# Optimization experiments

Measured on AMD Instinct MI355X. Metric: run time of the kernel, lower is better.

Reference implementation:

```python
import jax, jax.numpy as jnp
import numpy as np

ALPHA = 1.0

def setup_inputs() -> dict:
    key = jax.random.key(0)
    k1, k2, k3, k4 = jax.random.split(key, 4)
    B, N, D = 2048, 32768, 128
    return {
        "anchor": jax.random.normal(k1, (B, D), dtype=jnp.float32),
        "positive": jax.random.normal(k2, (B, D), dtype=jnp.float32),
        "negative": jax.random.normal(k3, (N, D), dtype=jnp.float32),
        "r_score": jax.random.normal(k4, (B, 1), dtype=jnp.float32),
    }

def reference(anchor, positive, negative, r_score):
    # pos_sim: [B,1] elementwise dot per row
    pos_sim = jnp.sum(anchor * positive, axis=1, keepdims=True)
    # neg_mul: [B,N] score matrix; row-wise stable logsumexp -> [B,1]
    neg_mul = jnp.matmul(anchor, negative.T)
    neg_sim = jax.scipy.special.logsumexp(neg_mul, axis=1, keepdims=True)
    loss = jax.nn.relu(neg_sim - pos_sim + r_score + ALPHA)
    return jnp.mean(loss)
```

## Files before the change

kernel.cpp:

```cpp
#include <hip/hip_runtime.h>
#include <hip/hip_bf16.h>


#define B_ROWS 2048
#define N_NEG  32768
#define DIM    128
#define LOG2E  1.4426950408889634f
#define LN2    0.6931471805599453f

typedef __bf16 bf16x8 __attribute__((ext_vector_type(8)));
typedef float  f32x4  __attribute__((ext_vector_type(4)));

static __device__ inline unsigned short f2bf(float f) {
    union { float f; unsigned u; } v; v.f = f;
    unsigned r = v.u + 0x7FFF + ((v.u >> 16) & 1);
    return (unsigned short)(r >> 16);
}

static __device__ inline void load_lds16(const void* g, void* s) {
    __builtin_amdgcn_global_load_lds(
        (const __attribute__((address_space(1))) void*)g,
        (__attribute__((address_space(3))) void*)s,
        16, 0, 0);
}

__global__ void prep(const float* __restrict__ anchor,
                     const float* __restrict__ positive,
                     const float* __restrict__ neg,
                     unsigned short* __restrict__ a_bf,
                     unsigned short* __restrict__ n_bf,
                     float* __restrict__ pos_sim,
                     float* __restrict__ sumexp) {
    int t = threadIdx.x;
    if (blockIdx.x < 256) {
        int row = blockIdx.x * 8 + (t >> 5);
        int c4  = (t & 31) * 4;
        const float4 a4 = *(const float4*)(anchor   + row * DIM + c4);
        const float4 p4 = *(const float4*)(positive + row * DIM + c4);
        float dot = a4.x * p4.x + a4.y * p4.y + a4.z * p4.z + a4.w * p4.w;
        ushort4 ab;
        ab.x = f2bf(a4.x * LOG2E); ab.y = f2bf(a4.y * LOG2E);
        ab.z = f2bf(a4.z * LOG2E); ab.w = f2bf(a4.w * LOG2E);
        *(ushort4*)(a_bf + row * DIM + c4) = ab;
        #pragma unroll
        for (int m = 1; m <= 16; m <<= 1) dot += __shfl_xor(dot, m, 64);
        if ((t & 31) == 0) { pos_sim[row] = dot; sumexp[row] = 0.0f; }
    } else {
        int i = (blockIdx.x - 256) * 256 + t;
        #pragma unroll
        for (int k = 0; k < 4; k++) {
            int idx = i + k * (1024 * 256);
            float4 v = *(const float4*)(neg + (size_t)idx * 4);
            ushort4 o;
            o.x = f2bf(v.x); o.y = f2bf(v.y); o.z = f2bf(v.z); o.w = f2bf(v.w);
            *(ushort4*)(n_bf + (size_t)idx * 4) = o;
        }
    }
}

#define CHUNK 1024
#define TSTEPS (CHUNK / 128)

__global__ __launch_bounds__(256, 2) void fused_gemm_lse(
        const unsigned short* __restrict__ A,
        const unsigned short* __restrict__ Nb,
        float* __restrict__ sumexp) {
    __shared__ unsigned short lds[4 * 8192];

    const int bid     = blockIdx.x;
    const int rowTile = bid & 15;
    const int chunk   = bid >> 4;
    const int wave = threadIdx.x >> 6, lane = threadIdx.x & 63;
    const int wr = wave >> 1, wc = wave & 1;
    const int q = lane >> 4, c = lane & 15;
    const int lrow = lane >> 4;
    const int lchk = lane & 15;

    const unsigned short* Ag = A + rowTile * (128 * DIM);
    const unsigned short* Bg = Nb + (size_t)(chunk * CHUNK) * DIM;

#define STAGE_TILE(gbase, tt)                                                  \
    {                                                                          \
        const int h_ = wave >> 1;                                              \
        const int s_ = (2 * (tt) + 2 + h_) & 3;                                \
        _Pragma("unroll")                                                      \
        for (int i_ = 0; i_ < 8; i_++) {                                       \
            int rloc_ = (wave & 1) * 32 + i_ * 4;        \
            int rg_   = h_ * 64 + rloc_ + lrow;         \
            int gofs_ = rg_ * DIM + ((lchk ^ (rg_ & 7)) << 3);                 \
            load_lds16((gbase) + gofs_, &lds[s_ * 8192 + rloc_ * DIM]);        \
        }                                                                      \
    }

    STAGE_TILE(Ag, -1);
    STAGE_TILE(Bg, 0);
    asm volatile("s_waitcnt vmcnt(8)" ::: "memory");
    __builtin_amdgcn_s_barrier();

    int swz[4];
    #pragma unroll
    for (int k = 0; k < 4; k++) swz[k] = (((k * 4 + q) ^ (c & 7)) << 3);

    bf16x8 af[4][4];
    #pragma unroll
    for (int i = 0; i < 4; i++) {
        int row = i * 16 + c;
        #pragma unroll
        for (int k = 0; k < 4; k++)
            af[i][k] = *(const bf16x8*)&lds[wr * 8192 + row * DIM + swz[k]];
    }
    asm volatile("s_waitcnt lgkmcnt(0)" ::: "memory");
    __builtin_amdgcn_s_barrier();

    STAGE_TILE(Bg + 128 * DIM, 1);

    const f32x4 zero4 = {0.f, 0.f, 0.f, 0.f};
    f32x4 sumacc[4] = {zero4, zero4, zero4, zero4};

    for (int t = 0; t < TSTEPS; t++) {
        if (t < TSTEPS - 1) asm volatile("s_waitcnt vmcnt(8)" ::: "memory");
        else                asm volatile("s_waitcnt vmcnt(0)" ::: "memory");
        __builtin_amdgcn_s_barrier();

        const int sb = (2 * t + 2 + wc) & 3;
        #pragma unroll
        for (int j = 0; j < 4; j++) {
            int brow = j * 16 + c;
            bf16x8 bf[4];
            #pragma unroll
            for (int k = 0; k < 4; k++)
                bf[k] = *(const bf16x8*)&lds[sb * 8192 + brow * DIM + swz[k]];
            #pragma unroll
            for (int i = 0; i < 4; i++) {
                f32x4 acc = __builtin_amdgcn_mfma_f32_16x16x32_bf16(af[i][0], bf[0], zero4, 0, 0, 0);
                acc = __builtin_amdgcn_mfma_f32_16x16x32_bf16(af[i][1], bf[1], acc, 0, 0, 0);
                acc = __builtin_amdgcn_mfma_f32_16x16x32_bf16(af[i][2], bf[2], acc, 0, 0, 0);
                acc = __builtin_amdgcn_mfma_f32_16x16x32_bf16(af[i][3], bf[3], acc, 0, 0, 0);
                sumacc[i][0] += __builtin_amdgcn_exp2f(acc[0]);
                sumacc[i][1] += __builtin_amdgcn_exp2f(acc[1]);
                sumacc[i][2] += __builtin_amdgcn_exp2f(acc[2]);
                sumacc[i][3] += __builtin_amdgcn_exp2f(acc[3]);
            }
        }
        asm volatile("s_waitcnt lgkmcnt(0)" ::: "memory");
        __builtin_amdgcn_s_barrier();
        if (t + 2 < TSTEPS)
            STAGE_TILE(Bg + (size_t)(t + 2) * 128 * DIM, t + 2);
    }
#undef STAGE_TILE

    #pragma unroll
    for (int i = 0; i < 4; i++) {
        #pragma unroll
        for (int r = 0; r < 4; r++) {
            float v = sumacc[i][r];
            v += __shfl_xor(v, 1, 64);
            v += __shfl_xor(v, 2, 64);
            v += __shfl_xor(v, 4, 64);
            v += __shfl_xor(v, 8, 64);
            if ((lane & 15) == 0) {
                int row = rowTile * 128 + wr * 64 + i * 16 + q * 4 + r;
                atomicAdd(&sumexp[row], v);
            }
        }
    }
}

__global__ void finalize(const float* __restrict__ sumexp,
                         const float* __restrict__ pos_sim,
                         const float* __restrict__ r_score,
                         float* __restrict__ out) {
    __shared__ float red[4];
    int t = threadIdx.x;
    float acc = 0.0f;
    #pragma unroll
    for (int i = 0; i < 8; i++) {
        int row = t + i * 256;
        float lse  = __log2f(sumexp[row]) * LN2;
        float loss = lse - pos_sim[row] + r_score[row] + 1.0f;
        acc += fmaxf(loss, 0.0f);
    }
    #pragma unroll
    for (int m = 1; m <= 32; m <<= 1) acc += __shfl_xor(acc, m, 64);
    if ((t & 63) == 0) red[t >> 6] = acc;
    __syncthreads();
    if (t == 0) out[0] = (red[0] + red[1] + red[2] + red[3]) * (1.0f / (float)B_ROWS);
}

extern "C" void kernel_launch(void* const* d_in, const int* in_sizes, int n_in,
                              void* d_out, int out_size, void* d_ws, size_t ws_size,
                              hipStream_t stream) {
    const float* anchor   = (const float*)d_in[0];
    const float* positive = (const float*)d_in[1];
    const float* negative = (const float*)d_in[2];
    const float* r_score  = (const float*)d_in[3];
    float* out = (float*)d_out;

    char* ws = (char*)d_ws;
    float* sumexp           = (float*)ws;
    float* pos_sim          = (float*)(ws + 8192);
    unsigned short* a_bf    = (unsigned short*)(ws + 16384);
    unsigned short* n_bf    = (unsigned short*)(ws + 16384 + 524288);

    prep<<<1280, 256, 0, stream>>>(anchor, positive, negative, a_bf, n_bf, pos_sim, sumexp);
    fused_gemm_lse<<<512, 256, 0, stream>>>(a_bf, n_bf, sumexp);
    finalize<<<1, 256, 0, stream>>>(sumexp, pos_sim, r_score, out);
}
```

Measured before the change: 95.29 us.

## Shrink B tiles to 64 rows with triple buffering and raise occupancy

Restructures the fused GEMM+logsumexp kernel so that each step stages 64 negative rows instead of 128. It uses a 3-slot rotating LDS ring (A tile in slot 0 initially, then reused for B) with prefetch distance 3, and cuts LDS from 64KB to 48KB so three blocks can fit per CU. The chunk size is halved to 512, doubling the grid to 1024 blocks to fill the GPU better. The tradeoff is smaller per-step work with more barriers, plus twice as many atomicAdds and A-tile loads across blocks.

```diff
diff --git a/kernel.cpp b/kernel.cpp
--- a/kernel.cpp
+++ b/kernel.cpp
@@ -58,14 +58,14 @@
     }
 }
 
-#define CHUNK 1024
-#define TSTEPS (CHUNK / 128)
-
-__global__ __launch_bounds__(256, 2) void fused_gemm_lse(
+#define CHUNK 512
+#define TSTEPS (CHUNK / 64)
+
+__global__ __launch_bounds__(256, 3) void fused_gemm_lse(
         const unsigned short* __restrict__ A,
         const unsigned short* __restrict__ Nb,
         float* __restrict__ sumexp) {
-    __shared__ unsigned short lds[4 * 8192];
+    __shared__ unsigned short lds[3 * 8192];
 
     const int bid     = blockIdx.x;
     const int rowTile = bid & 15;
@@ -79,22 +79,26 @@
     const unsigned short* Ag = A + rowTile * (128 * DIM);
     const unsigned short* Bg = Nb + (size_t)(chunk * CHUNK) * DIM;
 
-#define STAGE_TILE(gbase, tt)                                                  \
+#define STAGE_B(gbase, s_)                                                     \
     {                                                                          \
-        const int h_ = wave >> 1;                                              \
-        const int s_ = (2 * (tt) + 2 + h_) & 3;                                \
         _Pragma("unroll")                                                      \
-        for (int i_ = 0; i_ < 8; i_++) {                                       \
-            int rloc_ = (wave & 1) * 32 + i_ * 4;        \
-            int rg_   = h_ * 64 + rloc_ + lrow;         \
+        for (int i_ = 0; i_ < 4; i_++) {                                       \
+            int rloc_ = wave * 16 + i_ * 4;                                    \
+            int rg_   = rloc_ + lrow;                                          \
             int gofs_ = rg_ * DIM + ((lchk ^ (rg_ & 7)) << 3);                 \
-            load_lds16((gbase) + gofs_, &lds[s_ * 8192 + rloc_ * DIM]);        \
+            load_lds16((gbase) + gofs_, &lds[(s_) * 8192 + rloc_ * DIM]);      \
         }                                                                      \
     }
 
-    STAGE_TILE(Ag, -1);
-    STAGE_TILE(Bg, 0);
-    asm volatile("s_waitcnt vmcnt(8)" ::: "memory");
+    #pragma unroll
+    for (int i = 0; i < 8; i++) {
+        int rloc = wave * 32 + i * 4;
+        int rg   = rloc + lrow;
+        int gofs = rg * DIM + ((lchk ^ (rg & 7)) << 3);
+        load_lds16(Ag + gofs, &lds[rloc * DIM]);
+    }
+    STAGE_B(Bg, 2);
+    asm volatile("s_waitcnt vmcnt(4)" ::: "memory");
     __builtin_amdgcn_s_barrier();
 
     int swz[4];
@@ -104,32 +108,35 @@
     bf16x8 af[4][4];
     #pragma unroll
     for (int i = 0; i < 4; i++) {
-        int row = i * 16 + c;
+        int row = wr * 64 + i * 16 + c;
         #pragma unroll
         for (int k = 0; k < 4; k++)
-            af[i][k] = *(const bf16x8*)&lds[wr * 8192 + row * DIM + swz[k]];
+            af[i][k] = *(const bf16x8*)&lds[row * DIM + swz[k]];
     }
     asm volatile("s_waitcnt lgkmcnt(0)" ::: "memory");
     __builtin_amdgcn_s_barrier();
 
-    STAGE_TILE(Bg + 128 * DIM, 1);
+    STAGE_B(Bg + 1 * 64 * DIM, 0);
+    STAGE_B(Bg + 2 * 64 * DIM, 1);
 
     const f32x4 zero4 = {0.f, 0.f, 0.f, 0.f};
     f32x4 sumacc[4] = {zero4, zero4, zero4, zero4};
 
+    int slot = 2;
     for (int t = 0; t < TSTEPS; t++) {
-        if (t < TSTEPS - 1) asm volatile("s_waitcnt vmcnt(8)" ::: "memory");
-        else                asm volatile("s_waitcnt vmcnt(0)" ::: "memory");
+        if (t < TSTEPS - 2)       asm volatile("s_waitcnt vmcnt(8)" ::: "memory");
+        else if (t == TSTEPS - 2) asm volatile("s_waitcnt vmcnt(4)" ::: "memory");
+        else                      asm volatile("s_waitcnt vmcnt(0)" ::: "memory");
         __builtin_amdgcn_s_barrier();
 
-        const int sb = (2 * t + 2 + wc) & 3;
-        #pragma unroll
-        for (int j = 0; j < 4; j++) {
-            int brow = j * 16 + c;
+        const int sb = slot * 8192;
+        #pragma unroll
+        for (int j = 0; j < 2; j++) {
+            int brow = wc * 32 + j * 16 + c;
             bf16x8 bf[4];
             #pragma unroll
             for (int k = 0; k < 4; k++)
-                bf[k] = *(const bf16x8*)&lds[sb * 8192 + brow * DIM + swz[k]];
+                bf[k] = *(const bf16x8*)&lds[sb + brow * DIM + swz[k]];
             #pragma unroll
             for (int i = 0; i < 4; i++) {
                 f32x4 acc = __builtin_amdgcn_mfma_f32_16x16x32_bf16(af[i][0], bf[0], zero4, 0, 0, 0);
@@ -144,10 +151,11 @@
         }
         asm volatile("s_waitcnt lgkmcnt(0)" ::: "memory");
         __builtin_amdgcn_s_barrier();
-        if (t + 2 < TSTEPS)
-            STAGE_TILE(Bg + (size_t)(t + 2) * 128 * DIM, t + 2);
-    }
-#undef STAGE_TILE
+        if (t + 3 < TSTEPS)
+            STAGE_B(Bg + (size_t)(t + 3) * 64 * DIM, slot);
+        slot = (slot == 2) ? 0 : slot + 1;
+    }
+#undef STAGE_B
 
     #pragma unroll
     for (int i = 0; i < 4; i++) {
@@ -203,6 +211,6 @@
     unsigned short* n_bf    = (unsigned short*)(ws + 16384 + 524288);
 
     prep<<<1280, 256, 0, stream>>>(anchor, positive, negative, a_bf, n_bf, pos_sim, sumexp);
-    fused_gemm_lse<<<512, 256, 0, stream>>>(a_bf, n_bf, sumexp);
+    fused_gemm_lse<<<1024, 256, 0, stream>>>(a_bf, n_bf, sumexp);
     finalize<<<1, 256, 0, stream>>>(sumexp, pos_sim, r_score, out);
 }
```

After: 134.4 us. 41.0% more time.

## Swap GEMM roles: keep negatives in registers, stream all anchors through LDS

Applied to the files above, without the earlier changes.

Each block now owns a 64-row slice of negatives held in registers and streams all 2048 bf16 anchor rows through double-buffered LDS tiles, rather than holding a 128-row anchor tile and streaming 1024 negatives. Per-row exp-sums are written as per-block partials into an 8 MB buffer in place of atomics, then reduced by a new finalize kernel. This cuts global reads of the large negative matrix, since each negative is read once, but adds the partial write and read traffic and an extra launch. It also does one cross-lane reduction per tile, which adds shuffle work.

```diff
diff --git a/kernel.cpp b/kernel.cpp
--- a/kernel.cpp
+++ b/kernel.cpp
@@ -7,6 +7,7 @@
 #define DIM    128
 #define LOG2E  1.4426950408889634f
 #define LN2    0.6931471805599453f
+#define TSTEPS 16
 
 typedef __bf16 bf16x8 __attribute__((ext_vector_type(8)));
 typedef float  f32x4  __attribute__((ext_vector_type(4)));
@@ -58,42 +59,44 @@
     }
 }
 
-#define CHUNK 1024
-#define TSTEPS (CHUNK / 128)
-
 __global__ __launch_bounds__(256, 2) void fused_gemm_lse(
         const unsigned short* __restrict__ A,
         const unsigned short* __restrict__ Nb,
-        float* __restrict__ sumexp) {
-    __shared__ unsigned short lds[4 * 8192];
-
-    const int bid     = blockIdx.x;
-    const int rowTile = bid & 15;
-    const int chunk   = bid >> 4;
+        float* __restrict__ partial) {
+    __shared__ unsigned short lds[2 * 16384];
+
+    const int chunk = blockIdx.x;
     const int wave = threadIdx.x >> 6, lane = threadIdx.x & 63;
     const int wr = wave >> 1, wc = wave & 1;
     const int q = lane >> 4, c = lane & 15;
     const int lrow = lane >> 4;
     const int lchk = lane & 15;
 
-    const unsigned short* Ag = A + rowTile * (128 * DIM);
-    const unsigned short* Bg = Nb + (size_t)(chunk * CHUNK) * DIM;
-
-#define STAGE_TILE(gbase, tt)                                                  \
+    const unsigned short* Ag = A;
+    const unsigned short* Bg = Nb + (size_t)chunk * 64 * DIM;
+
+#define STAGE_A(tt, bsel)                                                      \
     {                                                                          \
-        const int h_ = wave >> 1;                                              \
-        const int s_ = (2 * (tt) + 2 + h_) & 3;                                \
+        const unsigned short* Gt_ = Ag + (size_t)(tt) * 128 * DIM;             \
         _Pragma("unroll")                                                      \
         for (int i_ = 0; i_ < 8; i_++) {                                       \
-            int rloc_ = (wave & 1) * 32 + i_ * 4;        \
-            int rg_   = h_ * 64 + rloc_ + lrow;         \
+            int rloc_ = wave * 32 + i_ * 4;                                    \
+            int rg_   = rloc_ + lrow;                                          \
             int gofs_ = rg_ * DIM + ((lchk ^ (rg_ & 7)) << 3);                 \
-            load_lds16((gbase) + gofs_, &lds[s_ * 8192 + rloc_ * DIM]);        \
+            load_lds16(Gt_ + gofs_, &lds[(bsel) * 16384 + rloc_ * DIM]);       \
         }                                                                      \
     }
 
-    STAGE_TILE(Ag, -1);
-    STAGE_TILE(Bg, 0);
+    bf16x8 bf[2][4];
+    #pragma unroll
+    for (int j = 0; j < 2; j++) {
+        const unsigned short* br = Bg + (size_t)(wc * 32 + j * 16 + c) * DIM;
+        #pragma unroll
+        for (int k = 0; k < 4; k++)
+            bf[j][k] = *(const bf16x8*)(br + (k * 4 + q) * 8);
+    }
+    STAGE_A(0, 0);
+    STAGE_A(1, 1);
     asm volatile("s_waitcnt vmcnt(8)" ::: "memory");
     __builtin_amdgcn_s_barrier();
 
@@ -101,75 +104,65 @@
     #pragma unroll
     for (int k = 0; k < 4; k++) swz[k] = (((k * 4 + q) ^ (c & 7)) << 3);
 
-    bf16x8 af[4][4];
-    #pragma unroll
-    for (int i = 0; i < 4; i++) {
-        int row = i * 16 + c;
-        #pragma unroll
-        for (int k = 0; k < 4; k++)
-            af[i][k] = *(const bf16x8*)&lds[wr * 8192 + row * DIM + swz[k]];
-    }
-    asm volatile("s_waitcnt lgkmcnt(0)" ::: "memory");
-    __builtin_amdgcn_s_barrier();
-
-    STAGE_TILE(Bg + 128 * DIM, 1);
-
     const f32x4 zero4 = {0.f, 0.f, 0.f, 0.f};
-    f32x4 sumacc[4] = {zero4, zero4, zero4, zero4};
+    float* Pp = partial + (size_t)(chunk * 2 + wc) * B_ROWS;
 
     for (int t = 0; t < TSTEPS; t++) {
         if (t < TSTEPS - 1) asm volatile("s_waitcnt vmcnt(8)" ::: "memory");
         else                asm volatile("s_waitcnt vmcnt(0)" ::: "memory");
         __builtin_amdgcn_s_barrier();
 
-        const int sb = (2 * t + 2 + wc) & 3;
-        #pragma unroll
-        for (int j = 0; j < 4; j++) {
-            int brow = j * 16 + c;
-            bf16x8 bf[4];
+        const int ab = (t & 1) * 16384;
+        #pragma unroll
+        for (int i = 0; i < 4; i++) {
+            int arow = wr * 64 + i * 16 + c;
+            bf16x8 af[4];
             #pragma unroll
             for (int k = 0; k < 4; k++)
-                bf[k] = *(const bf16x8*)&lds[sb * 8192 + brow * DIM + swz[k]];
+                af[k] = *(const bf16x8*)&lds[ab + arow * DIM + swz[k]];
+            f32x4 acc0 = __builtin_amdgcn_mfma_f32_16x16x32_bf16(bf[0][0], af[0], zero4, 0, 0, 0);
+            f32x4 acc1 = __builtin_amdgcn_mfma_f32_16x16x32_bf16(bf[1][0], af[0], zero4, 0, 0, 0);
             #pragma unroll
-            for (int i = 0; i < 4; i++) {
-                f32x4 acc = __builtin_amdgcn_mfma_f32_16x16x32_bf16(af[i][0], bf[0], zero4, 0, 0, 0);
-                acc = __builtin_amdgcn_mfma_f32_16x16x32_bf16(af[i][1], bf[1], acc, 0, 0, 0);
-                acc = __builtin_amdgcn_mfma_f32_16x16x32_bf16(af[i][2], bf[2], acc, 0, 0, 0);
-                acc = __builtin_amdgcn_mfma_f32_16x16x32_bf16(af[i][3], bf[3], acc, 0, 0, 0);
-                sumacc[i][0] += __builtin_amdgcn_exp2f(acc[0]);
-                sumacc[i][1] += __builtin_amdgcn_exp2f(acc[1]);
-                sumacc[i][2] += __builtin_amdgcn_exp2f(acc[2]);
-                sumacc[i][3] += __builtin_amdgcn_exp2f(acc[3]);
+            for (int k = 1; k < 4; k++) {
+                acc0 = __builtin_amdgcn_mfma_f32_16x16x32_bf16(bf[0][k], af[k], acc0, 0, 0, 0);
+                acc1 = __builtin_amdgcn_mfma_f32_16x16x32_bf16(bf[1][k], af[k], acc1, 0, 0, 0);
             }
+            float rs = __builtin_amdgcn_exp2f(acc0[0]) + __builtin_amdgcn_exp2f(acc0[1])
+                     + __builtin_amdgcn_exp2f(acc0[2]) + __builtin_amdgcn_exp2f(acc0[3])
+                     + __builtin_amdgcn_exp2f(acc1[0]) + __builtin_amdgcn_exp2f(acc1[1])
+                     + __builtin_amdgcn_exp2f(acc1[2]) + __builtin_amdgcn_exp2f(acc1[3]);
+            rs += __shfl_xor(rs, 16, 64);
+            rs += __shfl_xor(rs, 32, 64);
+            if (lane < 16)
+                Pp[t * 128 + wr * 64 + i * 16 + lane] = rs;
         }
         asm volatile("s_waitcnt lgkmcnt(0)" ::: "memory");
         __builtin_amdgcn_s_barrier();
-        if (t + 2 < TSTEPS)
-            STAGE_TILE(Bg + (size_t)(t + 2) * 128 * DIM, t + 2);
-    }
-#undef STAGE_TILE
-
-    #pragma unroll
-    for (int i = 0; i < 4; i++) {
-        #pragma unroll
-        for (int r = 0; r < 4; r++) {
-            float v = sumacc[i][r];
-            v += __shfl_xor(v, 1, 64);
-            v += __shfl_xor(v, 2, 64);
-            v += __shfl_xor(v, 4, 64);
-            v += __shfl_xor(v, 8, 64);
-            if ((lane & 15) == 0) {
-                int row = rowTile * 128 + wr * 64 + i * 16 + q * 4 + r;
-                atomicAdd(&sumexp[row], v);
-            }
-        }
-    }
-}
-
-__global__ void finalize(const float* __restrict__ sumexp,
-                         const float* __restrict__ pos_sim,
-                         const float* __restrict__ r_score,
-                         float* __restrict__ out) {
+        if (t + 2 < TSTEPS) STAGE_A(t + 2, t & 1);
+    }
+#undef STAGE_A
+}
+
+__global__ void finalizeA(const float* __restrict__ partial,
+                          float* __restrict__ sumexp) {
+    int r  = (blockIdx.x & 7) * 256 + threadIdx.x;
+    int cb = blockIdx.x >> 3;
+    const float* P = partial + (size_t)cb * 128 * B_ROWS + r;
+    float a0 = 0.f, a1 = 0.f, a2 = 0.f, a3 = 0.f;
+    #pragma unroll 4
+    for (int cidx = 0; cidx < 128; cidx += 4) {
+        a0 += P[(size_t)(cidx + 0) * B_ROWS];
+        a1 += P[(size_t)(cidx + 1) * B_ROWS];
+        a2 += P[(size_t)(cidx + 2) * B_ROWS];
+        a3 += P[(size_t)(cidx + 3) * B_ROWS];
+    }
+    atomicAdd(&sumexp[r], (a0 + a1) + (a2 + a3));
+}
+
+__global__ void finalizeB(const float* __restrict__ sumexp,
+                          const float* __restrict__ pos_sim,
+                          const float* __restrict__ r_score,
+                          float* __restrict__ out) {
     __shared__ float red[4];
     int t = threadIdx.x;
     float acc = 0.0f;
@@ -199,10 +192,12 @@
     char* ws = (char*)d_ws;
     float* sumexp           = (float*)ws;
     float* pos_sim          = (float*)(ws + 8192);
-    unsigned short* a_bf    = (unsigned short*)(ws + 16384);
-    unsigned short* n_bf    = (unsigned short*)(ws + 16384 + 524288);
+    float* partial          = (float*)(ws + 16384);
+    unsigned short* a_bf    = (unsigned short*)(ws + 16384 + 8388608);
+    unsigned short* n_bf    = (unsigned short*)(ws + 16384 + 8388608 + 524288);
 
     prep<<<1280, 256, 0, stream>>>(anchor, positive, negative, a_bf, n_bf, pos_sim, sumexp);
-    fused_gemm_lse<<<512, 256, 0, stream>>>(a_bf, n_bf, sumexp);
-    finalize<<<1, 256, 0, stream>>>(sumexp, pos_sim, r_score, out);
-}
+    fused_gemm_lse<<<512, 256, 0, stream>>>(a_bf, n_bf, partial);
+    finalizeA<<<64, 256, 0, stream>>>(partial, sumexp);
+    finalizeB<<<1, 256, 0, stream>>>(sumexp, pos_sim, r_score, out);
+}
```

Result: slower. 121.8 us (+27.8%).

## Fuse negative fp32-to-bf16 conversion into GEMM via fp32 LDS staging

Applied to the files above, without the earlier changes.

Removes the separate pass in prep that converted the 32768x128 negative matrix to bf16. The GEMM kernel now streams fp32 negative tiles (64 rows each) straight into LDS with a swizzled layout and converts them to bf16 in registers before the MFMA. This drops a full read and write of the negative matrix plus the bf16 reread. In exchange, each of the 16 row-tile blocks now reads the fp32 data (twice the bytes per block), does extra LDS reads and conversion work in the inner loop, and has a different buffering layout.

```diff
diff --git a/kernel.cpp b/kernel.cpp
--- a/kernel.cpp
+++ b/kernel.cpp
@@ -26,46 +26,32 @@
 
 __global__ void prep(const float* __restrict__ anchor,
                      const float* __restrict__ positive,
-                     const float* __restrict__ neg,
                      unsigned short* __restrict__ a_bf,
-                     unsigned short* __restrict__ n_bf,
                      float* __restrict__ pos_sim,
                      float* __restrict__ sumexp) {
     int t = threadIdx.x;
-    if (blockIdx.x < 256) {
-        int row = blockIdx.x * 8 + (t >> 5);
-        int c4  = (t & 31) * 4;
-        const float4 a4 = *(const float4*)(anchor   + row * DIM + c4);
-        const float4 p4 = *(const float4*)(positive + row * DIM + c4);
-        float dot = a4.x * p4.x + a4.y * p4.y + a4.z * p4.z + a4.w * p4.w;
-        ushort4 ab;
-        ab.x = f2bf(a4.x * LOG2E); ab.y = f2bf(a4.y * LOG2E);
-        ab.z = f2bf(a4.z * LOG2E); ab.w = f2bf(a4.w * LOG2E);
-        *(ushort4*)(a_bf + row * DIM + c4) = ab;
-        #pragma unroll
-        for (int m = 1; m <= 16; m <<= 1) dot += __shfl_xor(dot, m, 64);
-        if ((t & 31) == 0) { pos_sim[row] = dot; sumexp[row] = 0.0f; }
-    } else {
-        int i = (blockIdx.x - 256) * 256 + t;
-        #pragma unroll
-        for (int k = 0; k < 4; k++) {
-            int idx = i + k * (1024 * 256);
-            float4 v = *(const float4*)(neg + (size_t)idx * 4);
-            ushort4 o;
-            o.x = f2bf(v.x); o.y = f2bf(v.y); o.z = f2bf(v.z); o.w = f2bf(v.w);
-            *(ushort4*)(n_bf + (size_t)idx * 4) = o;
-        }
-    }
+    int row = blockIdx.x * 8 + (t >> 5);
+    int c4  = (t & 31) * 4;
+    const float4 a4 = *(const float4*)(anchor   + row * DIM + c4);
+    const float4 p4 = *(const float4*)(positive + row * DIM + c4);
+    float dot = a4.x * p4.x + a4.y * p4.y + a4.z * p4.z + a4.w * p4.w;
+    ushort4 ab;
+    ab.x = f2bf(a4.x * LOG2E); ab.y = f2bf(a4.y * LOG2E);
+    ab.z = f2bf(a4.z * LOG2E); ab.w = f2bf(a4.w * LOG2E);
+    *(ushort4*)(a_bf + row * DIM + c4) = ab;
+    #pragma unroll
+    for (int m = 1; m <= 16; m <<= 1) dot += __shfl_xor(dot, m, 64);
+    if ((t & 31) == 0) { pos_sim[row] = dot; sumexp[row] = 0.0f; }
 }
 
 #define CHUNK 1024
-#define TSTEPS (CHUNK / 128)
+#define TSTEPS (CHUNK / 64)
 
 __global__ __launch_bounds__(256, 2) void fused_gemm_lse(
         const unsigned short* __restrict__ A,
-        const unsigned short* __restrict__ Nb,
+        const float* __restrict__ Neg,
         float* __restrict__ sumexp) {
-    __shared__ unsigned short lds[4 * 8192];
+    __shared__ unsigned short lds[2 * 16384];
 
     const int bid     = blockIdx.x;
     const int rowTile = bid & 15;
@@ -77,24 +63,29 @@
     const int lchk = lane & 15;
 
     const unsigned short* Ag = A + rowTile * (128 * DIM);
-    const unsigned short* Bg = Nb + (size_t)(chunk * CHUNK) * DIM;
-
-#define STAGE_TILE(gbase, tt)                                                  \
+    const float* Bg = Neg + (size_t)(chunk * CHUNK) * DIM;
+
+#define STAGE_B(tt, bsel)                                                      \
     {                                                                          \
-        const int h_ = wave >> 1;                                              \
-        const int s_ = (2 * (tt) + 2 + h_) & 3;                                \
+        const float* Gt_ = Bg + (size_t)(tt) * 64 * DIM;                       \
         _Pragma("unroll")                                                      \
         for (int i_ = 0; i_ < 8; i_++) {                                       \
-            int rloc_ = (wave & 1) * 32 + i_ * 4;        \
-            int rg_   = h_ * 64 + rloc_ + lrow;         \
-            int gofs_ = rg_ * DIM + ((lchk ^ (rg_ & 7)) << 3);                 \
-            load_lds16((gbase) + gofs_, &lds[s_ * 8192 + rloc_ * DIM]);        \
+            int rbase_ = wave * 16 + i_ * 2;            \
+            int r_     = rbase_ + (lane >> 5);                                 \
+            int slot_  = lane & 31;                                            \
+            int gofs_  = r_ * DIM + ((slot_ ^ (r_ & 7)) << 2);                 \
+            load_lds16(Gt_ + gofs_, &lds[(bsel) * 16384 + rbase_ * 256]);      \
         }                                                                      \
     }
 
-    STAGE_TILE(Ag, -1);
-    STAGE_TILE(Bg, 0);
-    asm volatile("s_waitcnt vmcnt(8)" ::: "memory");
+    #pragma unroll
+    for (int i = 0; i < 8; i++) {
+        int off = wave * 4096 + i * 512;
+        int r   = (off >> 7) + lrow;
+        int gofs = r * DIM + ((lchk ^ (r & 7)) << 3);
+        load_lds16(Ag + gofs, &lds[off]);
+    }
+    asm volatile("s_waitcnt vmcnt(0)" ::: "memory");
     __builtin_amdgcn_s_barrier();
 
     int swz[4];
@@ -104,15 +95,16 @@
     bf16x8 af[4][4];
     #pragma unroll
     for (int i = 0; i < 4; i++) {
-        int row = i * 16 + c;
+        int row = wr * 64 + i * 16 + c;
         #pragma unroll
         for (int k = 0; k < 4; k++)
-            af[i][k] = *(const bf16x8*)&lds[wr * 8192 + row * DIM + swz[k]];
+            af[i][k] = *(const bf16x8*)&lds[row * DIM + swz[k]];
     }
     asm volatile("s_waitcnt lgkmcnt(0)" ::: "memory");
     __builtin_amdgcn_s_barrier();
 
-    STAGE_TILE(Bg + 128 * DIM, 1);
+    STAGE_B(0, 0);
+    STAGE_B(1, 1);
 
     const f32x4 zero4 = {0.f, 0.f, 0.f, 0.f};
     f32x4 sumacc[4] = {zero4, zero4, zero4, zero4};
@@ -122,14 +114,23 @@
         else                asm volatile("s_waitcnt vmcnt(0)" ::: "memory");
         __builtin_amdgcn_s_barrier();
 
-        const int sb = (2 * t + 2 + wc) & 3;
+        const int bb = (t & 1) * 16384;
         #pragma unroll
-        for (int j = 0; j < 4; j++) {
-            int brow = j * 16 + c;
+        for (int j = 0; j < 2; j++) {
+            int brow = wc * 32 + j * 16 + c;
             bf16x8 bf[4];
             #pragma unroll
-            for (int k = 0; k < 4; k++)
-                bf[k] = *(const bf16x8*)&lds[sb * 8192 + brow * DIM + swz[k]];
+            for (int k = 0; k < 4; k++) {
+                int slotA = (8 * k + 2 * q) ^ (c & 7);
+                const float4 fA = *(const float4*)&lds[bb + brow * 256 + slotA * 8];
+                const float4 fB = *(const float4*)&lds[bb + brow * 256 + (slotA ^ 1) * 8];
+                bf16x8 f;
+                f[0] = (__bf16)fA.x; f[1] = (__bf16)fA.y;
+                f[2] = (__bf16)fA.z; f[3] = (__bf16)fA.w;
+                f[4] = (__bf16)fB.x; f[5] = (__bf16)fB.y;
+                f[6] = (__bf16)fB.z; f[7] = (__bf16)fB.w;
+                bf[k] = f;
+            }
             #pragma unroll
             for (int i = 0; i < 4; i++) {
                 f32x4 acc = __builtin_amdgcn_mfma_f32_16x16x32_bf16(af[i][0], bf[0], zero4, 0, 0, 0);
@@ -144,10 +145,9 @@
         }
         asm volatile("s_waitcnt lgkmcnt(0)" ::: "memory");
         __builtin_amdgcn_s_barrier();
-        if (t + 2 < TSTEPS)
-            STAGE_TILE(Bg + (size_t)(t + 2) * 128 * DIM, t + 2);
-    }
-#undef STAGE_TILE
+        if (t + 2 < TSTEPS) STAGE_B(t + 2, t & 1);
+    }
+#undef STAGE_B
 
     #pragma unroll
     for (int i = 0; i < 4; i++) {
@@ -200,9 +200,8 @@
     float* sumexp           = (float*)ws;
     float* pos_sim          = (float*)(ws + 8192);
     unsigned short* a_bf    = (unsigned short*)(ws + 16384);
-    unsigned short* n_bf    = (unsigned short*)(ws + 16384 + 524288);
-
-    prep<<<1280, 256, 0, stream>>>(anchor, positive, negative, a_bf, n_bf, pos_sim, sumexp);
-    fused_gemm_lse<<<512, 256, 0, stream>>>(a_bf, n_bf, sumexp);
+
+    prep<<<256, 256, 0, stream>>>(anchor, positive, a_bf, pos_sim, sumexp);
+    fused_gemm_lse<<<512, 256, 0, stream>>>(a_bf, negative, sumexp);
     finalize<<<1, 256, 0, stream>>>(sumexp, pos_sim, r_score, out);
 }
```

Result: slower. 100.5 us (+5.5%).
